# Kernel optimization log

Hardware: AMD Instinct MI355X
Metric: run time of the kernel (lower is better)

Reference implementation:

```python
import jax, jax.numpy as jnp
import numpy as np

N_NODES = 100000
N_EDGES = 1600000
D_IN, D_H1, D_H2 = 128, 64, 16


def setup_inputs() -> dict:
    key = jax.random.key(0)
    ks = jax.random.split(key, 12)
    def glorot(k, shape):
        fan_in, fan_out = shape
        lim = np.sqrt(6.0 / (fan_in + fan_out)).astype(np.float32)
        return jax.random.uniform(k, shape, jnp.float32, -lim, lim)
    x = jax.random.normal(ks[0], (N_NODES, D_IN), jnp.float32)
    edge_index = jax.random.randint(ks[1], (2, N_EDGES), 0, N_NODES, jnp.int64)
    return {
        "x": x,
        "edge_index": edge_index,
        # SAGEConv1: lin_l (neighbor agg, has bias), lin_r (root, no bias) -- stored (in,out)
        "w1_l": glorot(ks[2], (D_IN, D_H1)),
        "w1_r": glorot(ks[3], (D_IN, D_H1)),
        "b1": jnp.zeros((D_H1,), jnp.float32),
        # SAGEConv2
        "w2_l": glorot(ks[4], (D_H1, D_H2)),
        "w2_r": glorot(ks[5], (D_H1, D_H2)),
        "b2": jnp.zeros((D_H2,), jnp.float32),
        # MLP head
        "fc1_w": glorot(ks[6], (D_H2, 8)),
        "fc1_b": jnp.zeros((8,), jnp.float32),
        "fc2_w": glorot(ks[7], (8, 1)),
        "fc2_b": jnp.zeros((1,), jnp.float32),
    }


def _sage_conv(h, src, dst, n_nodes, w_l, w_r, b):
    # mean aggregation of source-node features into destination nodes
    msgs = h[src]                                                  # [E, d]
    agg = jax.ops.segment_sum(msgs, dst, num_segments=n_nodes)     # [N, d]
    deg = jax.ops.segment_sum(jnp.ones((src.shape[0],), h.dtype), dst,
                              num_segments=n_nodes)                # [N]
    mean = agg / jnp.maximum(deg, 1.0)[:, None]
    return mean @ w_l + h @ w_r + b


def reference(x, edge_index, w1_l, w1_r, b1, w2_l, w2_r, b2,
              fc1_w, fc1_b, fc2_w, fc2_b):
    src, dst = edge_index[0], edge_index[1]
    n = x.shape[0]
    h = _sage_conv(x, src, dst, n, w1_l, w1_r, b1)   # [N, 64]
    h = _sage_conv(h, src, dst, n, w2_l, w2_r, b2)   # [N, 16]
    # embedding_mlp on edge endpoint embeddings
    e = h[src] * h[dst]                              # [E, 16]
    out = (e @ fc1_w + fc1_b) @ fc2_w + fc2_b        # [E, 1]
    return jax.nn.sigmoid(out)
```

## Files before the change

kernel.cpp:

```cpp
#include <hip/hip_runtime.h>
#include <hip/hip_fp16.h>
#include <math.h>

#define NN 100000
#define NE 1600000

#define BSH  9
#define BKN  512
#define NB   196
#define ABLK 256
#define EPB  ((NE + ABLK - 1) / ABLK)
#define GEMMB ((NN + 63) / 64)
#define GBLK ((GEMMB + 1) / 2)
#define LDST 136

typedef __attribute__((ext_vector_type(8))) short bf16x8;
typedef __attribute__((ext_vector_type(4))) float f32x4;

__device__ __forceinline__ unsigned short f2bf(float f) {
    unsigned u = __builtin_bit_cast(unsigned, f);
    u += 0x7fffu + ((u >> 16) & 1u);
    return (unsigned short)(u >> 16);
}
__device__ __forceinline__ float bf2f(unsigned short h) {
    unsigned u = ((unsigned)h) << 16;
    return __builtin_bit_cast(float, u);
}
__device__ __forceinline__ float2 unpackh2(unsigned w) {
    const __half2 h = __builtin_bit_cast(__half2, w);
    return __half22float2(h);
}

struct GemmSmem { unsigned short sAh[64 * LDST]; unsigned short sAl[64 * LDST]; };
struct ScatSmem { int cur[NB]; int tot[NB]; int sarr[512]; };
union F1Smem { GemmSmem gm; ScatSmem sc; };

__global__ __launch_bounds__(256) void fused0(const int* __restrict__ dst,
    const float* __restrict__ w1l, const float* __restrict__ w1r,
    const float* __restrict__ w2l, const float* __restrict__ w2r,
    const float* __restrict__ b1, const float* __restrict__ fc1w,
    const float* __restrict__ fc1b, const float* __restrict__ fc2w,
    const float* __restrict__ fc2b, int* __restrict__ mat,
    unsigned short* __restrict__ ATh, unsigned short* __restrict__ ATl,
    float* __restrict__ cbuf)
{
    __shared__ int h[NB];
    __shared__ float sl[64], sr[64];
    const int t = threadIdx.x;
    if (blockIdx.x < ABLK) {
        for (int i = t; i < NB; i += 256) h[i] = 0;
        __syncthreads();
        const int a = blockIdx.x;
        const int beg = a * EPB;
        const int end = (beg + EPB < NE) ? beg + EPB : NE;
        int e = beg + t;
        for (; e + 3 * 256 < end; e += 4 * 256) {
            const int d0 = dst[e], d1 = dst[e + 256], d2 = dst[e + 512], d3 = dst[e + 768];
            atomicAdd(&h[d0 >> BSH], 1);
            atomicAdd(&h[d1 >> BSH], 1);
            atomicAdd(&h[d2 >> BSH], 1);
            atomicAdd(&h[d3 >> BSH], 1);
        }
        for (; e < end; e += 256)
            atomicAdd(&h[dst[e] >> BSH], 1);
        __syncthreads();
        for (int i = t; i < NB; i += 256) mat[(size_t)i * ABLK + a] = h[i];
        return;
    }
    if (blockIdx.x < ABLK + 128) {
        const int k = blockIdx.x - ABLK;
        const int j = t;
        if (j < 64) { sl[j] = w1l[k * 64 + j]; sr[j] = w1r[k * 64 + j]; }
        __syncthreads();
        if (j < 64) {
            const int sel = j >> 4, jj = j & 15;
            const float* row = (sel < 2) ? sl : sr;
            const float* w2  = (sel & 1) ? w2r : w2l;
            float acc = 0.f;
#pragma unroll
            for (int m = 0; m < 64; ++m) acc = fmaf(row[m], w2[m * 16 + jj], acc);
            const unsigned short hh = f2bf(acc);
            ATh[j * 128 + k] = hh;
            ATl[j * 128 + k] = f2bf(acc - bf2f(hh));
        }
        return;
    }
    const int j = t;
    if (j < 16) {
        float a = 0.f;
        for (int m = 0; m < 64; ++m) a = fmaf(b1[m], w2l[m * 16 + j], a);
        cbuf[j] = a;
    } else if (j < 32) {
        const int jj = j - 16;
        float a = 0.f;
        for (int m = 0; m < 64; ++m) a = fmaf(b1[m], w2r[m * 16 + jj], a);
        cbuf[j] = a;
    } else if (j < 48) {
        const int k = j - 32;
        float a = 0.f;
        for (int m = 0; m < 8; ++m) a = fmaf(fc1w[k * 8 + m], fc2w[m], a);
        cbuf[j] = a;
    } else if (j == 48) {
        float a = fc2b[0];
        for (int m = 0; m < 8; ++m) a = fmaf(fc1b[m], fc2w[m], a);
        cbuf[48] = a;
    }
}

__global__ __launch_bounds__(512) void fused1(const int* __restrict__ src,
    const int* __restrict__ dst, const int* __restrict__ mat,
    int* __restrict__ bbase, unsigned* __restrict__ part,
    const float* __restrict__ x, const unsigned short* __restrict__ ATh,
    const unsigned short* __restrict__ ATl, signed char* __restrict__ p8,
    float* __restrict__ pscale, __half* __restrict__ qh)
{
    __shared__ F1Smem su;
    const int tid = threadIdx.x;

    if (blockIdx.x < ABLK) {
        int* cur  = su.sc.cur;
        int* tot  = su.sc.tot;
        int* sarr = su.sc.sarr;
        const int a = blockIdx.x;
        for (int i = tid; i < NB; i += 512) {
            const int* col = mat + (size_t)i * ABLK;
            int run = 0, mypre = 0;
            for (int a2 = 0; a2 < ABLK; ++a2) {
                const int v = col[a2];
                mypre += (a2 < a) ? v : 0;
                run += v;
            }
            tot[i] = run;
            cur[i] = mypre;
        }
        __syncthreads();
        const int myrun = (tid < NB) ? tot[tid] : 0;
        sarr[tid] = myrun;
        __syncthreads();
        for (int off = 1; off < 512; off <<= 1) {
            const int u = (tid >= off) ? sarr[tid - off] : 0;
            __syncthreads();
            sarr[tid] += u;
            __syncthreads();
        }
        if (tid < NB) {
            const int base = sarr[tid] - myrun;
            cur[tid] += base;
            if (a == 0) bbase[tid] = base;
        }
        if (a == 0 && tid == NB - 1) bbase[NB] = sarr[tid];
        __syncthreads();

        const int beg = a * EPB;
        const int end = (beg + EPB < NE) ? beg + EPB : NE;
        int e = beg + tid;
        for (; e + 3 * 512 < end; e += 4 * 512) {
            const int s0 = src[e],          d0 = dst[e];
            const int s1 = src[e + 512],    d1 = dst[e + 512];
            const int s2 = src[e + 1024],   d2 = dst[e + 1024];
            const int s3 = src[e + 1536],   d3 = dst[e + 1536];
            const int p0 = atomicAdd(&cur[d0 >> BSH], 1);
            const int p1 = atomicAdd(&cur[d1 >> BSH], 1);
            const int p2 = atomicAdd(&cur[d2 >> BSH], 1);
            const int p3 = atomicAdd(&cur[d3 >> BSH], 1);
            part[p0] = ((unsigned)s0 << BSH) | (unsigned)(d0 & (BKN - 1));
            part[p1] = ((unsigned)s1 << BSH) | (unsigned)(d1 & (BKN - 1));
            part[p2] = ((unsigned)s2 << BSH) | (unsigned)(d2 & (BKN - 1));
            part[p3] = ((unsigned)s3 << BSH) | (unsigned)(d3 & (BKN - 1));
        }
        for (; e < end; e += 512) {
            const int s = src[e], d = dst[e];
            const int pos = atomicAdd(&cur[d >> BSH], 1);
            part[pos] = ((unsigned)s << BSH) | (unsigned)(d & (BKN - 1));
        }
        return;
    }

    unsigned short* sAh = su.gm.sAh;
    unsigned short* sAl = su.gm.sAl;
    for (int i = tid; i < 1024; i += 512) {
        const int row = i >> 4, ch = i & 15;
        const uint4 vh = *(const uint4*)(ATh + row * 128 + ch * 8);
        const uint4 vl = *(const uint4*)(ATl + row * 128 + ch * 8);
        *(uint4*)(sAh + row * LDST + ch * 8) = vh;
        *(uint4*)(sAl + row * LDST + ch * 8) = vl;
    }
    __syncthreads();

    const int wave8 = tid >> 6;
    const int tile = (blockIdx.x - ABLK) * 2 + (wave8 >> 2);
    const int wave = wave8 & 3;
    const int lane = tid & 63;
    const int lr = lane & 15;
    const int lg = lane >> 4;

    bf16x8 bh[4][4], bl[4][4];
#pragma unroll
    for (int ct = 0; ct < 4; ++ct) {
        const int col = ct * 16 + lr;
#pragma unroll
        for (int ks = 0; ks < 4; ++ks) {
            const int k0 = ks * 32 + lg * 8;
            bh[ct][ks] = *(const bf16x8*)(sAh + col * LDST + k0);
            bl[ct][ks] = *(const bf16x8*)(sAl + col * LDST + k0);
        }
    }

    if (tile >= GEMMB) return;
    const int tilebase = tile * 64;
    const int xrowidx = tilebase + wave * 16 + lr;
    const float* xrow = x + (size_t)(xrowidx < NN ? xrowidx : NN - 1) * 128;

    f32x4 acc[4] = {f32x4{0,0,0,0}, f32x4{0,0,0,0}, f32x4{0,0,0,0}, f32x4{0,0,0,0}};
#pragma unroll
    for (int ks = 0; ks < 4; ++ks) {
        const int k0 = ks * 32 + lg * 8;
        const float4 v0 = *(const float4*)(xrow + k0);
        const float4 v1 = *(const float4*)(xrow + k0 + 4);
        const float vv[8] = {v0.x, v0.y, v0.z, v0.w, v1.x, v1.y, v1.z, v1.w};
        bf16x8 xh, xl;
#pragma unroll
        for (int j = 0; j < 8; ++j) {
            const unsigned short h = f2bf(vv[j]);
            xh[j] = (short)h;
            xl[j] = (short)f2bf(vv[j] - bf2f(h));
        }
#pragma unroll
        for (int ct = 0; ct < 4; ++ct) {
            acc[ct] = __builtin_amdgcn_mfma_f32_16x16x32_bf16(xh, bh[ct][ks], acc[ct], 0, 0, 0);
            acc[ct] = __builtin_amdgcn_mfma_f32_16x16x32_bf16(xh, bl[ct][ks], acc[ct], 0, 0, 0);
            acc[ct] = __builtin_amdgcn_mfma_f32_16x16x32_bf16(xl, bh[ct][ks], acc[ct], 0, 0, 0);
        }
    }

#pragma unroll
    for (int rg = 0; rg < 4; ++rg) {
        float m = fmaxf(fabsf(acc[0][rg]), fabsf(acc[1][rg]));
#pragma unroll
        for (int d = 1; d < 16; d <<= 1) m = fmaxf(m, __shfl_xor(m, d, 64));
        m = fmaxf(m, 1e-20f);
        const float scl = m * (1.0f / 127.0f);
        const float inv = 127.0f / m;
        const int nrow = tilebase + wave * 16 + lg * 4 + rg;
        if (nrow < NN) {
            const int q0 = __float2int_rn(acc[0][rg] * inv);
            const int q1 = __float2int_rn(acc[1][rg] * inv);
            p8[(size_t)nrow * 32 + lr]      = (signed char)q0;
            p8[(size_t)nrow * 32 + 16 + lr] = (signed char)q1;
            if (lr == 0) pscale[nrow] = scl;
            qh[(size_t)nrow * 32 + lr]      = __float2half(acc[2][rg]);
            qh[(size_t)nrow * 32 + 16 + lr] = __float2half(acc[3][rg]);
        }
    }
}

__global__ __launch_bounds__(512) void partB_build(const unsigned* __restrict__ part,
    const int* __restrict__ bbase, int* __restrict__ rowptr, int* __restrict__ cols)
{
    __shared__ int h[BKN];
    __shared__ int cur[BKN];
    __shared__ int wsum[8];
    const int b = blockIdx.x;
    const int t = threadIdx.x;
    const int beg = bbase[b], end = bbase[b + 1];
    h[t] = 0;
    __syncthreads();
    {
        int e = beg + t;
        for (; e + 3 * 512 < end; e += 4 * 512) {
            const unsigned w0 = part[e], w1 = part[e + 512];
            const unsigned w2 = part[e + 1024], w3 = part[e + 1536];
            atomicAdd(&h[w0 & (BKN - 1u)], 1);
            atomicAdd(&h[w1 & (BKN - 1u)], 1);
            atomicAdd(&h[w2 & (BKN - 1u)], 1);
            atomicAdd(&h[w3 & (BKN - 1u)], 1);
        }
        for (; e < end; e += 512)
            atomicAdd(&h[part[e] & (BKN - 1u)], 1);
    }
    __syncthreads();
    const int v = h[t];
    int inc = v;
#pragma unroll
    for (int d = 1; d < 64; d <<= 1) {
        const int u = __shfl_up(inc, d, 64);
        if ((t & 63) >= d) inc += u;
    }
    if ((t & 63) == 63) wsum[t >> 6] = inc;
    __syncthreads();
    int woff = 0;
    for (int w = 0; w < (t >> 6); ++w) woff += wsum[w];
    const int excl = inc + woff - v;
    cur[t] = excl;
    const int node = b * BKN + t;
    if (node < NN) rowptr[node] = beg + excl;
    if (b == NB - 1 && t == 0) rowptr[NN] = NE;
    __syncthreads();
    {
        int e = beg + t;
        for (; e + 3 * 512 < end; e += 4 * 512) {
            const unsigned w0 = part[e], w1 = part[e + 512];
            const unsigned w2 = part[e + 1024], w3 = part[e + 1536];
            const int p0 = atomicAdd(&cur[w0 & (BKN - 1u)], 1);
            const int p1 = atomicAdd(&cur[w1 & (BKN - 1u)], 1);
            const int p2 = atomicAdd(&cur[w2 & (BKN - 1u)], 1);
            const int p3 = atomicAdd(&cur[w3 & (BKN - 1u)], 1);
            cols[beg + p0] = (int)(w0 >> BSH);
            cols[beg + p1] = (int)(w1 >> BSH);
            cols[beg + p2] = (int)(w2 >> BSH);
            cols[beg + p3] = (int)(w3 >> BSH);
        }
        for (; e < end; e += 512) {
            const unsigned w = part[e];
            const int pos = atomicAdd(&cur[w & (BKN - 1u)], 1);
            cols[beg + pos] = (int)(w >> BSH);
        }
    }
}

__global__ __launch_bounds__(256) void agg1_csr(const int* __restrict__ rowptr,
    const int* __restrict__ cols, const signed char* __restrict__ p8,
    const float* __restrict__ pscale, const __half* __restrict__ qh,
    const float* __restrict__ cbuf, __half* __restrict__ g, __half* __restrict__ r)
{
    const int node = blockIdx.x * 8 + (threadIdx.x >> 5);
    if (node >= NN) return;
    const int lane = threadIdx.x & 31;
    const int es = lane >> 2;
    const int k  = lane & 3;
    const int beg = rowptr[node], end = rowptr[node + 1];
    const int deg = end - beg;
    const int grpbase = threadIdx.x & 32;
    const int myc = (lane < deg) ? cols[beg + lane] : 0;
    const uint2* p64 = (const uint2*)p8;
    float a0 = 0.f, a1 = 0.f, a2 = 0.f, a3 = 0.f;
    float a4 = 0.f, a5 = 0.f, a6 = 0.f, a7 = 0.f;
#pragma unroll 2
    for (int base = 0; base < deg; base += 8) {
        const int idx = base + es;
        const bool valid = idx < deg;
        int s;
        if (idx < 32) s = __shfl(myc, grpbase + idx, 64);
        else          s = cols[beg + (valid ? idx : deg - 1)];
        const float scl = valid ? pscale[s] : 0.f;
        const uint2 w = p64[(size_t)s * 4 + k];
        a0 = fmaf((float)(signed char)(w.x & 0xffu), scl, a0);
        a1 = fmaf((float)(signed char)((w.x >> 8) & 0xffu), scl, a1);
        a2 = fmaf((float)(signed char)((w.x >> 16) & 0xffu), scl, a2);
        a3 = fmaf((float)(signed char)(w.x >> 24), scl, a3);
        a4 = fmaf((float)(signed char)(w.y & 0xffu), scl, a4);
        a5 = fmaf((float)(signed char)((w.y >> 8) & 0xffu), scl, a5);
        a6 = fmaf((float)(signed char)((w.y >> 16) & 0xffu), scl, a6);
        a7 = fmaf((float)(signed char)(w.y >> 24), scl, a7);
    }
#pragma unroll
    for (int d = 4; d <= 16; d <<= 1) {
        a0 += __shfl_xor(a0, d, 64); a1 += __shfl_xor(a1, d, 64);
        a2 += __shfl_xor(a2, d, 64); a3 += __shfl_xor(a3, d, 64);
        a4 += __shfl_xor(a4, d, 64); a5 += __shfl_xor(a5, d, 64);
        a6 += __shfl_xor(a6, d, 64); a7 += __shfl_xor(a7, d, 64);
    }
    if (es == 0) {
        const float dg = (float)deg;
        const float inv = 1.0f / fmaxf(dg, 1.0f);
        const uint4 qw = *(const uint4*)(qh + (size_t)node * 32 + 8 * k);
        const float2 q0 = unpackh2(qw.x), q1 = unpackh2(qw.y);
        const float2 q2 = unpackh2(qw.z), q3 = unpackh2(qw.w);
        const float4 cb0 = *(const float4*)(cbuf + 8 * k);
        const float4 cb1 = *(const float4*)(cbuf + 8 * k + 4);
        const float v0 = fmaf(a0, inv, q0.x + cb0.x);
        const float v1 = fmaf(a1, inv, q0.y + cb0.y);
        const float v2 = fmaf(a2, inv, q1.x + cb0.z);
        const float v3 = fmaf(a3, inv, q1.y + cb0.w);
        const float v4 = fmaf(a4, inv, q2.x + cb1.x);
        const float v5 = fmaf(a5, inv, q2.y + cb1.y);
        const float v6 = fmaf(a6, inv, q3.x + cb1.z);
        const float v7 = fmaf(a7, inv, q3.y + cb1.w);
        uint4 ow;
        ow.x = __builtin_bit_cast(unsigned, __floats2half2_rn(v0, v1));
        ow.y = __builtin_bit_cast(unsigned, __floats2half2_rn(v2, v3));
        ow.z = __builtin_bit_cast(unsigned, __floats2half2_rn(v4, v5));
        ow.w = __builtin_bit_cast(unsigned, __floats2half2_rn(v6, v7));
        if (k < 2) *(uint4*)(g + (size_t)node * 16 + 8 * k) = ow;
        else       *(uint4*)(r + (size_t)node * 16 + 8 * (k - 2)) = ow;
    }
}

__global__ __launch_bounds__(256) void agg2_csr(const int* __restrict__ rowptr,
    const int* __restrict__ cols, const __half* __restrict__ g,
    const __half* __restrict__ r, const float* __restrict__ b2,
    __half* __restrict__ h2)
{
    const int node = blockIdx.x * 8 + (threadIdx.x >> 5);
    if (node >= NN) return;
    const int lane = threadIdx.x & 31;
    const int es = lane >> 2;
    const int k  = lane & 3;
    const int beg = rowptr[node], end = rowptr[node + 1];
    const int deg = end - beg;
    const int grpbase = threadIdx.x & 32;
    const int myc = (lane < deg) ? cols[beg + lane] : 0;
    const uint2* g64 = (const uint2*)g;
    float a0 = 0.f, a1 = 0.f, a2 = 0.f, a3 = 0.f;
#pragma unroll 2
    for (int base = 0; base < deg; base += 8) {
        const int idx = base + es;
        const bool valid = idx < deg;
        int s;
        if (idx < 32) s = __shfl(myc, grpbase + idx, 64);
        else          s = cols[beg + (valid ? idx : deg - 1)];
        const float m = valid ? 1.0f : 0.0f;
        const uint2 w = g64[(size_t)s * 4 + k];
        const float2 v0 = unpackh2(w.x);
        const float2 v1 = unpackh2(w.y);
        a0 = fmaf(v0.x, m, a0);
        a1 = fmaf(v0.y, m, a1);
        a2 = fmaf(v1.x, m, a2);
        a3 = fmaf(v1.y, m, a3);
    }
#pragma unroll
    for (int d = 4; d <= 16; d <<= 1) {
        a0 += __shfl_xor(a0, d, 64); a1 += __shfl_xor(a1, d, 64);
        a2 += __shfl_xor(a2, d, 64); a3 += __shfl_xor(a3, d, 64);
    }
    if (es == 0) {
        const float dg = (float)deg;
        const float inv = 1.0f / fmaxf(dg, 1.0f);
        const uint2 rw = ((const uint2*)r)[(size_t)node * 4 + k];
        const float2 r0 = unpackh2(rw.x), r1 = unpackh2(rw.y);
        const float4 bb = *(const float4*)(b2 + 4 * k);
        const float v0 = fmaf(a0, inv, r0.x + bb.x);
        const float v1 = fmaf(a1, inv, r0.y + bb.y);
        const float v2 = fmaf(a2, inv, r1.x + bb.z);
        const float v3 = fmaf(a3, inv, r1.y + bb.w);
        uint2 ow;
        ow.x = __builtin_bit_cast(unsigned, __floats2half2_rn(v0, v1));
        ow.y = __builtin_bit_cast(unsigned, __floats2half2_rn(v2, v3));
        ((uint2*)h2)[(size_t)node * 4 + k] = ow;
    }
}

__global__ __launch_bounds__(256) void edge_mlp(const int* __restrict__ src,
    const int* __restrict__ dst, const __half* __restrict__ h2,
    const float* __restrict__ cbuf, float* __restrict__ out)
{
    __shared__ float sv[17];
    if (threadIdx.x < 16) sv[threadIdx.x] = cbuf[32 + threadIdx.x];
    if (threadIdx.x == 16) sv[16] = cbuf[48];
    __syncthreads();
    const int e0 = (blockIdx.x * 256 + threadIdx.x) * 4;
    if (e0 + 3 < NE) {
        const int4 s4 = *(const int4*)(src + e0);
        const int4 d4 = *(const int4*)(dst + e0);
        const int ss[4] = {s4.x, s4.y, s4.z, s4.w};
        const int dd[4] = {d4.x, d4.y, d4.z, d4.w};
        float4 res;
        float* resp = (float*)&res;
#pragma unroll
        for (int u = 0; u < 4; ++u) {
            const uint4* hs = (const uint4*)(h2 + (size_t)ss[u] * 16);
            const uint4* hd = (const uint4*)(h2 + (size_t)dd[u] * 16);
            const uint4 a0 = hs[0], a1 = hs[1];
            const uint4 b0 = hd[0], b1 = hd[1];
            const unsigned aw[8] = {a0.x, a0.y, a0.z, a0.w, a1.x, a1.y, a1.z, a1.w};
            const unsigned bw[8] = {b0.x, b0.y, b0.z, b0.w, b1.x, b1.y, b1.z, b1.w};
            float acc = sv[16];
#pragma unroll
            for (int qq = 0; qq < 8; ++qq) {
                const float2 a = unpackh2(aw[qq]);
                const float2 b = unpackh2(bw[qq]);
                acc = fmaf(a.x * b.x, sv[qq * 2 + 0], acc);
                acc = fmaf(a.y * b.y, sv[qq * 2 + 1], acc);
            }
            resp[u] = 1.0f / (1.0f + __expf(-acc));
        }
        *(float4*)(out + e0) = res;
    } else {
        for (int e = e0; e < NE; ++e) {
            const int s = src[e], d = dst[e];
            const uint4* hs = (const uint4*)(h2 + (size_t)s * 16);
            const uint4* hd = (const uint4*)(h2 + (size_t)d * 16);
            const uint4 a0 = hs[0], a1 = hs[1];
            const uint4 b0 = hd[0], b1 = hd[1];
            const unsigned aw[8] = {a0.x, a0.y, a0.z, a0.w, a1.x, a1.y, a1.z, a1.w};
            const unsigned bw[8] = {b0.x, b0.y, b0.z, b0.w, b1.x, b1.y, b1.z, b1.w};
            float acc = sv[16];
#pragma unroll
            for (int qq = 0; qq < 8; ++qq) {
                const float2 a = unpackh2(aw[qq]);
                const float2 b = unpackh2(bw[qq]);
                acc = fmaf(a.x * b.x, sv[qq * 2 + 0], acc);
                acc = fmaf(a.y * b.y, sv[qq * 2 + 1], acc);
            }
            out[e] = 1.0f / (1.0f + __expf(-acc));
        }
    }
}

extern "C" void kernel_launch(void* const* d_in, const int* in_sizes, int n_in,
                              void* d_out, int out_size, void* d_ws, size_t ws_size,
                              hipStream_t stream)
{
    const float* x    = (const float*)d_in[0];
    const int*   ei   = (const int*)d_in[1];
    const float* w1l  = (const float*)d_in[2];
    const float* w1r  = (const float*)d_in[3];
    const float* b1   = (const float*)d_in[4];
    const float* w2l  = (const float*)d_in[5];
    const float* w2r  = (const float*)d_in[6];
    const float* b2   = (const float*)d_in[7];
    const float* fc1w = (const float*)d_in[8];
    const float* fc1b = (const float*)d_in[9];
    const float* fc2w = (const float*)d_in[10];
    const float* fc2b = (const float*)d_in[11];
    float* out = (float*)d_out;

    const int* src = ei;
    const int* dst = ei + NE;

    int* W = (int*)d_ws;
    size_t o = 0;
#define ALIGN16() o = (o + 15) & ~(size_t)15
    int* mat    = W + o; o += (size_t)NB * ABLK; ALIGN16();
    int* bbase  = W + o; o += NB + 1;            ALIGN16();
    int* rowptr = W + o; o += NN + 1;            ALIGN16();
    unsigned* part = (unsigned*)(W + o); o += NE; ALIGN16();
    int* cols   = W + o; o += NE;                ALIGN16();
    unsigned short* ATh = (unsigned short*)(W + o); o += 4096; ALIGN16();
    unsigned short* ATl = (unsigned short*)(W + o); o += 4096; ALIGN16();
    float* cbuf = (float*)(W + o); o += 64;      ALIGN16();
    signed char* p8 = (signed char*)(W + o); o += (size_t)NN * 8;  ALIGN16();
    float* pscale   = (float*)(W + o); o += NN;  ALIGN16();
    __half* qh  = (__half*)(W + o); o += (size_t)NN * 16; ALIGN16();
    __half* g   = (__half*)(W + o); o += (size_t)NN * 8;  ALIGN16();
    __half* r   = (__half*)(W + o); o += (size_t)NN * 8;  ALIGN16();
    __half* h2  = (__half*)(W + o); o += (size_t)NN * 8;  ALIGN16();

    fused0<<<ABLK + 129, 256, 0, stream>>>(dst, w1l, w1r, w2l, w2r, b1,
                                           fc1w, fc1b, fc2w, fc2b, mat, ATh, ATl, cbuf);
    fused1<<<ABLK + GBLK, 512, 0, stream>>>(src, dst, mat, bbase, part,
                                            x, ATh, ATl, p8, pscale, qh);
    partB_build<<<NB, 512, 0, stream>>>(part, bbase, rowptr, cols);
    agg1_csr<<<(NN + 7) / 8, 256, 0, stream>>>(rowptr, cols, p8, pscale, qh, cbuf, g, r);
    agg2_csr<<<(NN + 7) / 8, 256, 0, stream>>>(rowptr, cols, g, r, b2, h2);
    edge_mlp<<<(NE + 1023) / 1024, 256, 0, stream>>>(src, dst, h2, cbuf, out);
}
```

Measured before the change: 120.8 us.

## Prefetch gathered feature tables into cache and vectorize prefix column scan

```diff
diff --git a/kernel.cpp b/kernel.cpp
--- a/kernel.cpp
+++ b/kernel.cpp
@@ -123,12 +123,17 @@
         int* sarr = su.sc.sarr;
         const int a = blockIdx.x;
         for (int i = tid; i < NB; i += 512) {
-            const int* col = mat + (size_t)i * ABLK;
+            const int4* col4 = (const int4*)(mat + (size_t)i * ABLK);
             int run = 0, mypre = 0;
-            for (int a2 = 0; a2 < ABLK; ++a2) {
-                const int v = col[a2];
-                mypre += (a2 < a) ? v : 0;
-                run += v;
+#pragma unroll 4
+            for (int q = 0; q < ABLK / 4; ++q) {
+                const int4 v = col4[q];
+                const int b0 = q * 4;
+                run += v.x + v.y + v.z + v.w;
+                mypre += (b0 + 0 < a) ? v.x : 0;
+                mypre += (b0 + 1 < a) ? v.y : 0;
+                mypre += (b0 + 2 < a) ? v.z : 0;
+                mypre += (b0 + 3 < a) ? v.w : 0;
             }
             tot[i] = run;
             cur[i] = mypre;
@@ -323,6 +328,20 @@
     const float* __restrict__ pscale, const __half* __restrict__ qh,
     const float* __restrict__ cbuf, __half* __restrict__ g, __half* __restrict__ r)
 {
+    if (blockIdx.x < 448) {
+        const int4* pre = (const int4*)p8;
+        const int slice = blockIdx.x >> 3;
+        int accx = 0;
+#pragma unroll
+        for (int i = 0; i < 16; ++i) {
+            const int idx = slice * 4096 + i * 256 + (int)threadIdx.x;
+            if (idx < 225000) {
+                const int4 v = pre[idx];
+                accx ^= v.x ^ v.y ^ v.z ^ v.w;
+            }
+        }
+        asm volatile("" :: "v"(accx));
+    }
     const int node = blockIdx.x * 8 + (threadIdx.x >> 5);
     if (node >= NN) return;
     const int lane = threadIdx.x & 31;
@@ -391,6 +410,20 @@
     const __half* __restrict__ r, const float* __restrict__ b2,
     __half* __restrict__ h2)
 {
+    if (blockIdx.x < 400) {
+        const int4* pre = (const int4*)g;
+        const int slice = blockIdx.x >> 3;
+        int accx = 0;
+#pragma unroll
+        for (int i = 0; i < 16; ++i) {
+            const int idx = slice * 4096 + i * 256 + (int)threadIdx.x;
+            if (idx < 200000) {
+                const int4 v = pre[idx];
+                accx ^= v.x ^ v.y ^ v.z ^ v.w;
+            }
+        }
+        asm volatile("" :: "v"(accx));
+    }
     const int node = blockIdx.x * 8 + (threadIdx.x >> 5);
     if (node >= NN) return;
     const int lane = threadIdx.x & 31;
```

Measured after the change: 123.4 us. 1.02x slower.
